# Kernel tuning notes

Hardware: AMD Instinct MI355X
Metric: run time of the kernel (lower is better)

Reference implementation:

```python
import jax, jax.numpy as jnp
import numpy as np

N_NODES = 10000
N_EDGES = 640000
D_IN = 128
D_OUT = 128


def setup_inputs() -> dict:
    key = jax.random.key(0)
    k1, k2, k3, k4 = jax.random.split(key, 4)
    x = jax.random.normal(k1, (N_NODES, D_IN), dtype=jnp.float32)
    # PyG GCNConv weight: [dim_out, dim_in] (glorot)
    W = jax.random.normal(k2, (D_OUT, D_IN), dtype=jnp.float32) * (1.0 / np.sqrt(D_IN))
    b = jnp.zeros((D_OUT,), dtype=jnp.float32)
    edge_weight = jax.random.uniform(k3, (N_EDGES,), dtype=jnp.float32)
    edge_index = jax.random.randint(k4, (2, N_EDGES), 0, N_NODES, dtype=jnp.int32)
    return {"x": x, "W": W, "b": b, "edge_weight": edge_weight, "edge_index": edge_index}


def reference(x, W, b, edge_weight, edge_index):
    N = x.shape[0]
    # --- add self loops (fill weight = 1.0), PyG default ---
    loops = jnp.arange(N, dtype=edge_index.dtype)
    src = jnp.concatenate([edge_index[0], loops])
    dst = jnp.concatenate([edge_index[1], loops])
    ew = jnp.concatenate([edge_weight, jnp.ones((N,), dtype=edge_weight.dtype)])
    # --- symmetric GCN normalization: deg from target index ---
    deg = jax.ops.segment_sum(ew, dst, num_segments=N)
    dinv = jnp.where(deg > 0, jax.lax.rsqrt(deg), 0.0)
    norm = dinv[src] * ew * dinv[dst]  # [E+N]
    # --- linear transform then gather-scale-scatter aggregation ---
    h = x @ W.T  # [N, D_OUT]
    msgs = h[src] * norm[:, None]  # [E+N, D_OUT]
    out = jax.ops.segment_sum(msgs, dst, num_segments=N)
    return out + b
```

## Files before the change

### kernel.cpp

```cpp
#include <hip/hip_runtime.h>

#define N_NODES 10000
#define N_EDGES 640000
#define D 128
#define CAP 128

typedef unsigned long long ull;
typedef unsigned short u16;
typedef unsigned int u32;

#define CHUNKS 512
#define EPC 1250
#define NR 500
#define RW 20
#define GEMM_NPB 32
#define GEMM_BLOCKS ((N_NODES + GEMM_NPB - 1) / GEMM_NPB)
#define SMEM_K1 16384
#define EWFX 262144.0f
#define EWM  0x1ffffffu

__device__ __forceinline__ u16 f2bf(float f) {
    unsigned u = __float_as_uint(f);
    unsigned r = (u + 0x7fffu + ((u >> 16) & 1u)) >> 16;
    return (u16)r;
}


__global__ void __launch_bounds__(256) k_bucket(
    const int* __restrict__ src, const int* __restrict__ dst,
    const float* __restrict__ ew, const float* __restrict__ x,
    const float* __restrict__ W, u16* __restrict__ h_bf,
    ull* __restrict__ grecs, u32* __restrict__ offs)
{
    extern __shared__ char smem[];
    const int t = threadIdx.x;

    if (blockIdx.x < CHUNKS) {
        u32* rcnt   = (u32*)smem;
        u32* ping   = (u32*)(smem + 2048);
        u32* pong   = (u32*)(smem + 4096);
        ull* sorted = (ull*)(smem + 6144);

        for (int i = t; i < 512; i += 256) rcnt[i] = 0;
        __syncthreads();

        const int e0 = blockIdx.x * EPC;
        u32 rs[5]; ull rec[5];
        #pragma unroll
        for (int i = 0; i < 5; ++i) {
            int idx = i * 256 + t;
            rs[i] = 0xffffffffu;
            if (idx < EPC) {
                int e = e0 + idx;
                int d = dst[e];
                int s = src[e];
                float w = ew[e];
                int r = d / RW;
                int bin = d - r * RW;
                u32 slot = atomicAdd(&rcnt[r], 1u);
                rs[i] = ((u32)r << 11) | slot;
                rec[i] = ((ull)__float_as_uint(w) << 32) | ((u32)s << 5) | (u32)bin;
            }
        }
        __syncthreads();

        u32* a = ping; u32* bq = pong;
        for (int i = t; i < 512; i += 256) a[i] = rcnt[i];
        __syncthreads();
        for (int dd = 1; dd < 512; dd <<= 1) {
            for (int i = t; i < 512; i += 256)
                bq[i] = a[i] + ((i >= dd) ? a[i - dd] : 0u);
            __syncthreads();
            u32* tmp = a; a = bq; bq = tmp;
        }

        #pragma unroll
        for (int i = 0; i < 5; ++i) {
            if (rs[i] != 0xffffffffu) {
                int r = (int)(rs[i] >> 11);
                int slot = (int)(rs[i] & 2047u);
                sorted[a[r] - rcnt[r] + slot] = rec[i];
            }
        }
        __syncthreads();

        {
            const uint4* sp = (const uint4*)sorted;
            uint4* gp = (uint4*)(grecs + (size_t)blockIdx.x * EPC);
            for (int i = t; i < EPC / 2; i += 256) gp[i] = sp[i];
            u32* ob = offs + (size_t)blockIdx.x * 512;
            for (int i = t; i < NR; i += 256) ob[i] = a[i] - rcnt[i];
            if (t == 0) ob[NR] = EPC;
        }
    } else {
        float* xs = (float*)smem;
        const int node0 = (blockIdx.x - CHUNKS) * GEMM_NPB;
        const int col = t & 127;
        const int half = t >> 7;

        #pragma unroll
        for (int r = 0; r < 16; ++r) {
            int row = half * 16 + r;
            int n = node0 + row;
            xs[row * D + col] = (n < N_NODES) ? x[n * D + col] : 0.0f;
        }
        __syncthreads();

        float acc[16];
        #pragma unroll
        for (int r = 0; r < 16; ++r) acc[r] = 0.0f;

        const float4* Wrow = (const float4*)&W[col * D];
        const float* xbase = &xs[half * 16 * D];
        for (int k4 = 0; k4 < D / 4; ++k4) {
            float4 w = Wrow[k4];
            int k = k4 * 4;
            #pragma unroll
            for (int r = 0; r < 16; ++r) {
                acc[r] += xbase[r * D + k + 0] * w.x;
                acc[r] += xbase[r * D + k + 1] * w.y;
                acc[r] += xbase[r * D + k + 2] * w.z;
                acc[r] += xbase[r * D + k + 3] * w.w;
            }
        }
        #pragma unroll
        for (int r = 0; r < 16; ++r) {
            int n = node0 + half * 16 + r;
            if (n < N_NODES) h_bf[n * D + col] = f2bf(acc[r]);
        }
    }
}


__global__ void __launch_bounds__(512) k_csr(
    const ull* __restrict__ grecs, const u32* __restrict__ offs,
    u32* __restrict__ gpacked, float* __restrict__ dinv, ull* __restrict__ csr)
{
    __shared__ u32 bcnt[RW];
    const int t = threadIdx.x;
    const int r = blockIdx.x;

    if (t < RW) bcnt[t] = 0;

    const u32* ob = offs + (size_t)t * 512;
    u32 o0 = ob[r], o1 = ob[r + 1];
    if (o0 > EPC) o0 = EPC;
    if (o1 > EPC) o1 = EPC;
    int cnt = (int)o1 - (int)o0;
    if (cnt < 0) cnt = 0;
    if (cnt > 64) cnt = 64;
    __syncthreads();

    const ull* seg = grecs + (size_t)t * EPC + o0;
    for (int j = 0; j < cnt; ++j) {
        ull v = seg[j];
        u32 lo = (u32)v;
        int bin = (int)(lo & 31u);
        u32 srcn = lo >> 5;
        u32 wb = (u32)(v >> 32);
        float w = __uint_as_float(wb);
        u32 add = (1u << 25) | (u32)(w * EWFX);
        u32 old = atomicAdd(&bcnt[bin], add);
        int pos = (int)(old >> 25);
        if (pos < CAP) {
            int dstg = r * RW + bin;
            csr[(size_t)dstg * CAP + pos] = ((ull)wb << 32) | srcn;
        }
    }
    __syncthreads();

    if (t < RW) {
        int n = r * RW + t;
        u32 v = bcnt[t];
        gpacked[n] = v;
        dinv[n] = rsqrtf(1.0f + (float)(v & EWM) * 0x1p-18f);
    }
}


#define AGG_NPB 4

__global__ void __launch_bounds__(256) k_agg(
    const u32* __restrict__ gpacked, const float* __restrict__ dinv,
    const ull* __restrict__ csr, const u16* __restrict__ h_bf,
    const float* __restrict__ b, float* __restrict__ out)
{
    const int wid  = threadIdx.x >> 6;
    const int lane = threadIdx.x & 63;
    const int n = blockIdx.x * AGG_NPB + wid;

    __shared__ ull sm[AGG_NPB][CAP];

    const int deg = (int)(gpacked[n] >> 25);
    const float dn = dinv[n];
    const ull* bucket = csr + (size_t)n * CAP;

    #pragma unroll
    for (int r = 0; r < 2; ++r) {
        int j = r * 64 + lane;
        if (j < deg) {
            ull v = bucket[j];
            int s = (int)(u32)(v & 0xffffffffu);
            float w = __uint_as_float((u32)(v >> 32));
            float nm = dinv[s] * w * dn;
            sm[wid][j] = ((ull)__float_as_uint(nm) << 32) | (u32)s;
        }
    }
    __syncthreads();

    float acc0 = 0.0f, acc1 = 0.0f;
    const ull* smw = sm[wid];
    #pragma unroll 4
    for (int j = 0; j < deg; ++j) {
        ull v = smw[j];
        int s = (int)(u32)v;
        float nm = __uint_as_float((u32)(v >> 32));
        u32 hc = *(const u32*)(h_bf + (size_t)s * D + lane * 2);
        acc0 += __uint_as_float(hc << 16) * nm;
        acc1 += __uint_as_float(hc & 0xffff0000u) * nm;
    }

    float s2 = dn * dn;
    u32 hs = *(const u32*)(h_bf + (size_t)n * D + lane * 2);
    acc0 += __uint_as_float(hs << 16) * s2;
    acc1 += __uint_as_float(hs & 0xffff0000u) * s2;
    float2 bb = *(const float2*)(b + lane * 2);
    float2 o;
    o.x = acc0 + bb.x;
    o.y = acc1 + bb.y;
    *(float2*)(out + (size_t)n * D + lane * 2) = o;
}


extern "C" void kernel_launch(void* const* d_in, const int* in_sizes, int n_in,
                              void* d_out, int out_size, void* d_ws, size_t ws_size,
                              hipStream_t stream) {
    const float* x  = (const float*)d_in[0];
    const float* W  = (const float*)d_in[1];
    const float* b  = (const float*)d_in[2];
    const float* ew = (const float*)d_in[3];
    const int* ei   = (const int*)d_in[4];
    const int* src = ei;
    const int* dst = ei + N_EDGES;
    float* out = (float*)d_out;

    char* ws = (char*)d_ws;
    u32*   gpacked = (u32*)(ws);
    float* dinv    = (float*)(ws + 40000);
    u16*   h_bf    = (u16*)(ws + 80000);
    ull*   csr     = (ull*)(ws + 2640000);
    ull*   grecs   = (ull*)(ws + 12880000);
    u32*   offs    = (u32*)(ws + 18000000);

    k_bucket<<<CHUNKS + GEMM_BLOCKS, 256, SMEM_K1, stream>>>(
        src, dst, ew, x, W, h_bf, grecs, offs);
    k_csr<<<NR, 512, 0, stream>>>(grecs, offs, gpacked, dinv, csr);
    k_agg<<<N_NODES / AGG_NPB, 256, 0, stream>>>(gpacked, dinv, csr, h_bf, b, out);
}
```

Measured before the change: 116.9 us.

## Fuse CSR construction into aggregation using per-range shared-memory buckets

The global CSR buffer is removed. A dinv-only pass now computes degrees, and a new range kernel re-reads the bucketed edge records, builds each 20-node range's adjacency list with precomputed normalization in shared memory, and then aggregates the bf16 features directly. This avoids writing and re-reading a scattered 10 MB CSR array and one separate normalization step. In exchange, the grouped records are read twice. Aggregation now runs in only 500 blocks, with 8 waves each covering 20 nodes unevenly, which lowers parallelism for the latency-bound gather.

```diff
diff --git a/kernel.cpp b/kernel.cpp
--- a/kernel.cpp
+++ b/kernel.cpp
@@ -132,9 +132,9 @@
 }
 
 
-__global__ void __launch_bounds__(512) k_csr(
+__global__ void __launch_bounds__(512) k_dinv(
     const ull* __restrict__ grecs, const u32* __restrict__ offs,
-    u32* __restrict__ gpacked, float* __restrict__ dinv, ull* __restrict__ csr)
+    u32* __restrict__ gpacked, float* __restrict__ dinv)
 {
     __shared__ u32 bcnt[RW];
     const int t = threadIdx.x;
@@ -154,18 +154,9 @@
     const ull* seg = grecs + (size_t)t * EPC + o0;
     for (int j = 0; j < cnt; ++j) {
         ull v = seg[j];
-        u32 lo = (u32)v;
-        int bin = (int)(lo & 31u);
-        u32 srcn = lo >> 5;
-        u32 wb = (u32)(v >> 32);
-        float w = __uint_as_float(wb);
-        u32 add = (1u << 25) | (u32)(w * EWFX);
-        u32 old = atomicAdd(&bcnt[bin], add);
-        int pos = (int)(old >> 25);
-        if (pos < CAP) {
-            int dstg = r * RW + bin;
-            csr[(size_t)dstg * CAP + pos] = ((ull)wb << 32) | srcn;
-        }
+        int bin = (int)((u32)v & 31u);
+        float w = __uint_as_float((u32)(v >> 32));
+        atomicAdd(&bcnt[bin], (1u << 25) | (u32)(w * EWFX));
     }
     __syncthreads();
 
@@ -178,57 +169,73 @@
 }
 
 
-#define AGG_NPB 4
-
-__global__ void __launch_bounds__(256) k_agg(
-    const u32* __restrict__ gpacked, const float* __restrict__ dinv,
-    const ull* __restrict__ csr, const u16* __restrict__ h_bf,
+__global__ void __launch_bounds__(512) k_range(
+    const ull* __restrict__ grecs, const u32* __restrict__ offs,
+    const float* __restrict__ dinv, const u16* __restrict__ h_bf,
     const float* __restrict__ b, float* __restrict__ out)
 {
-    const int wid  = threadIdx.x >> 6;
-    const int lane = threadIdx.x & 63;
-    const int n = blockIdx.x * AGG_NPB + wid;
-
-    __shared__ ull sm[AGG_NPB][CAP];
-
-    const int deg = (int)(gpacked[n] >> 25);
-    const float dn = dinv[n];
-    const ull* bucket = csr + (size_t)n * CAP;
-
-    #pragma unroll
-    for (int r = 0; r < 2; ++r) {
-        int j = r * 64 + lane;
-        if (j < deg) {
-            ull v = bucket[j];
-            int s = (int)(u32)(v & 0xffffffffu);
-            float w = __uint_as_float((u32)(v >> 32));
-            float nm = dinv[s] * w * dn;
-            sm[wid][j] = ((ull)__float_as_uint(nm) << 32) | (u32)s;
-        }
-    }
-    __syncthreads();
-
-    float acc0 = 0.0f, acc1 = 0.0f;
-    const ull* smw = sm[wid];
-    #pragma unroll 4
-    for (int j = 0; j < deg; ++j) {
-        ull v = smw[j];
-        int s = (int)(u32)v;
-        float nm = __uint_as_float((u32)(v >> 32));
-        u32 hc = *(const u32*)(h_bf + (size_t)s * D + lane * 2);
-        acc0 += __uint_as_float(hc << 16) * nm;
-        acc1 += __uint_as_float(hc & 0xffff0000u) * nm;
-    }
-
-    float s2 = dn * dn;
-    u32 hs = *(const u32*)(h_bf + (size_t)n * D + lane * 2);
-    acc0 += __uint_as_float(hs << 16) * s2;
-    acc1 += __uint_as_float(hs & 0xffff0000u) * s2;
+    __shared__ ull csr_s[RW * CAP];
+    __shared__ u32 bcnt[RW];
+    __shared__ float ldin[RW];
+    const int t = threadIdx.x;
+    const int r = blockIdx.x;
+
+    if (t < RW) {
+        bcnt[t] = 0;
+        ldin[t] = dinv[r * RW + t];
+    }
+
+    const u32* ob = offs + (size_t)t * 512;
+    u32 o0 = ob[r], o1 = ob[r + 1];
+    if (o0 > EPC) o0 = EPC;
+    if (o1 > EPC) o1 = EPC;
+    int cnt = (int)o1 - (int)o0;
+    if (cnt < 0) cnt = 0;
+    if (cnt > 64) cnt = 64;
+    __syncthreads();
+
+    const ull* seg = grecs + (size_t)t * EPC + o0;
+    for (int j = 0; j < cnt; ++j) {
+        ull v = seg[j];
+        u32 lo = (u32)v;
+        int bin = (int)(lo & 31u);
+        int s = (int)(lo >> 5);
+        float w = __uint_as_float((u32)(v >> 32));
+        float nm = dinv[s] * w * ldin[bin];
+        u32 pos = atomicAdd(&bcnt[bin], 1u);
+        if (pos < CAP)
+            csr_s[bin * CAP + pos] = ((ull)__float_as_uint(nm) << 32) | (u32)s;
+    }
+    __syncthreads();
+
+    const int wid  = t >> 6;
+    const int lane = t & 63;
     float2 bb = *(const float2*)(b + lane * 2);
-    float2 o;
-    o.x = acc0 + bb.x;
-    o.y = acc1 + bb.y;
-    *(float2*)(out + (size_t)n * D + lane * 2) = o;
+    for (int bin = wid; bin < RW; bin += 8) {
+        const int n = r * RW + bin;
+        int cnt2 = (int)bcnt[bin];
+        if (cnt2 > CAP) cnt2 = CAP;
+        float acc0 = 0.0f, acc1 = 0.0f;
+        const ull* cl = csr_s + bin * CAP;
+        #pragma unroll 4
+        for (int j = 0; j < cnt2; ++j) {
+            ull v = cl[j];
+            int s = (int)(u32)v;
+            float nm = __uint_as_float((u32)(v >> 32));
+            u32 hc = *(const u32*)(h_bf + (size_t)s * D + lane * 2);
+            acc0 += __uint_as_float(hc << 16) * nm;
+            acc1 += __uint_as_float(hc & 0xffff0000u) * nm;
+        }
+        float dn = ldin[bin];
+        float s2 = dn * dn;
+        u32 hs = *(const u32*)(h_bf + (size_t)n * D + lane * 2);
+        acc0 += __uint_as_float(hs << 16) * s2;
+        acc1 += __uint_as_float(hs & 0xffff0000u) * s2;
+        float2 o;
+        o.x = acc0 + bb.x;
+        o.y = acc1 + bb.y;
+        *(float2*)(out + (size_t)n * D + lane * 2) = o;
+    }
 }
 
 
@@ -248,12 +255,11 @@
     u32*   gpacked = (u32*)(ws);
     float* dinv    = (float*)(ws + 40000);
     u16*   h_bf    = (u16*)(ws + 80000);
-    ull*   csr     = (ull*)(ws + 2640000);
-    ull*   grecs   = (ull*)(ws + 12880000);
-    u32*   offs    = (u32*)(ws + 18000000);
+    ull*   grecs   = (ull*)(ws + 2640000);
+    u32*   offs    = (u32*)(ws + 7760000);
 
     k_bucket<<<CHUNKS + GEMM_BLOCKS, 256, SMEM_K1, stream>>>(
         src, dst, ew, x, W, h_bf, grecs, offs);
-    k_csr<<<NR, 512, 0, stream>>>(grecs, offs, gpacked, dinv, csr);
-    k_agg<<<N_NODES / AGG_NPB, 256, 0, stream>>>(gpacked, dinv, csr, h_bf, b, out);
-}
+    k_dinv<<<NR, 512, 0, stream>>>(grecs, offs, gpacked, dinv);
+    k_range<<<NR, 512, 0, stream>>>(grecs, offs, dinv, h_bf, b, out);
+}
```

Result: slower. 127.3 us (+8.8%).
